# Kernel tuning notes

Measured on AMD Instinct MI355X. Metric: run time of the kernel, lower is better.

## Reference

```python
import jax, jax.numpy as jnp
import numpy as np

V, E, H, OUT, T = 100000, 300, 512, 1, 2048


def setup_inputs() -> dict:
    key = jax.random.key(0)
    ks = jax.random.split(key, 15)
    s = 0.04  # ~1/sqrt(hidden) init scale
    return {
        "sentA": jax.random.randint(ks[0], (T,), 0, V),
        "sentB": jax.random.randint(ks[1], (T,), 0, V),
        "hidden": jnp.zeros((2, 2, H), jnp.float32),  # unused by forward, kept for signature fidelity
        "emb": jax.random.normal(ks[2], (V, E), jnp.float32) * 0.1,
        "w_ih": jax.random.normal(ks[3], (2, 4 * H, E), jnp.float32) * s,
        "w_hh": jax.random.normal(ks[4], (2, 4 * H, H), jnp.float32) * s,
        "b_ih": jax.random.normal(ks[5], (2, 4 * H), jnp.float32) * s,
        "b_hh": jax.random.normal(ks[6], (2, 4 * H), jnp.float32) * s,
        "bi_w": jax.random.uniform(ks[7], (1, 2), jnp.float32, -0.5, 0.5),
        "bi_b": jax.random.normal(ks[8], (1,), jnp.float32) * s,
        "blA": jax.random.uniform(ks[9], (H, H), jnp.float32, -0.1, 0.1),
        "blB": jax.random.uniform(ks[10], (H, H), jnp.float32, -0.1, 0.1),
        "bl_b": jax.random.normal(ks[11], (H,), jnp.float32) * s,
        "out_w": jax.random.uniform(ks[12], (OUT, H), jnp.float32, -0.1, 0.1),
        "out_b": jax.random.normal(ks[13], (OUT,), jnp.float32) * s,
    }


def _lstm_dir(x, w_ih, w_hh, b_ih, b_hh):
    # x: [T, E]; single-direction LSTM, returns final hidden state h_T [H]
    gx = x @ w_ih.T + (b_ih + b_hh)  # [T, 4H] input-gate preactivations, hoisted out of scan
    h_dim = w_hh.shape[1]

    def step(carry, g_t):
        h, c = carry
        g = g_t + h @ w_hh.T  # [4H]
        i, f, gg, o = jnp.split(g, 4, axis=-1)  # PyTorch gate order: i, f, g, o
        c = jax.nn.sigmoid(f) * c + jax.nn.sigmoid(i) * jnp.tanh(gg)
        h = jax.nn.sigmoid(o) * jnp.tanh(c)
        return (h, c), None

    init = (jnp.zeros((h_dim,), x.dtype), jnp.zeros((h_dim,), x.dtype))
    (h, _), _ = jax.lax.scan(step, init, gx)
    return h


def _encode(sent, emb, w_ih, w_hh, b_ih, b_hh, bi_w, bi_b):
    x = emb[sent]  # [T, E]
    h_fwd = _lstm_dir(x, w_ih[0], w_hh[0], b_ih[0], b_hh[0])
    h_bwd = _lstm_dir(x[::-1], w_ih[1], w_hh[1], b_ih[1], b_hh[1])
    hid = jnp.stack([h_fwd, h_bwd])  # [2, H]
    # bi_weight(hid.t()).t(): mixes the 2 directions per hidden unit -> [1, H]
    return bi_w @ hid + bi_b


def reference(sentA, sentB, hidden, emb, w_ih, w_hh, b_ih, b_hh,
              bi_w, bi_b, blA, blB, bl_b, out_w, out_b):
    hA = _encode(sentA, emb, w_ih, w_hh, b_ih, b_hh, bi_w, bi_b)  # [1, H]
    hB = _encode(sentB, emb, w_ih, w_hh, b_ih, b_hh, bi_w, bi_b)  # [1, H]
    # Double_Linear: A @ WA + B @ WB + bias
    biout = hA @ blA + hB @ blB + bl_b  # [1, H]
    out_l = jnp.tanh(biout) @ out_w.T + out_b  # [1, OUT]
    return jax.nn.sigmoid(out_l)
```

## Files before the change

kernel.cpp:

```cpp
#include <hip/hip_runtime.h>
#include <hip/hip_bf16.h>

#define T_LEN 2048
#define E_DIM 300
#define H_DIM 512
#define G_DIM 2048
#define NBLK  32
#define UPB   16
#define TAG_OFF 0x40000000u

#define WS_H   0
#define WS_X   16384
#define WS_GX  5242880

typedef float v2f __attribute__((ext_vector_type(2)));

__device__ __forceinline__ float sigmoid_fast(float x) {
    return 1.f / (1.f + __expf(-x));
}
__device__ __forceinline__ float tanh_fast(float x) {
    x = fminf(fmaxf(x, -15.f), 15.f);
    float e = __expf(-2.f * x);
    return (1.f - e) / (1.f + e);
}

__global__ void k_gather(const int* __restrict__ sentA, const int* __restrict__ sentB,
                         const float* __restrict__ emb, float* __restrict__ x) {
    const int s = blockIdx.y;
    const int* sent = s ? sentB : sentA;
    const int t0 = blockIdx.x * 16;
    for (int idx = threadIdx.x; idx < 16 * 300; idx += 256) {
        int r = idx / 300, e = idx - r * 300;
        int t = t0 + r;
        int row = sent[t];
        x[((size_t)(s * 2048 + t)) * 300 + e] = emb[(size_t)row * 300 + e];
    }
}

__global__ __launch_bounds__(256) void k_gemm(const float* __restrict__ x,
                                              const float* __restrict__ w_ih,
                                              const float* __restrict__ b_ih,
                                              const float* __restrict__ b_hh,
                                              __hip_bfloat16* __restrict__ gx) {
    __shared__ float xs[32 * 108];
    __shared__ float ws_[64 * 108];
    const int gi = blockIdx.x, ti = blockIdx.y, z = blockIdx.z;
    const int d = z >> 1, s = z & 1;
    const int t0 = ti * 32, g0 = gi * 64;
    const int tg = threadIdx.x & 15, tt = threadIdx.x >> 4;
    const float* wbase = w_ih + (size_t)d * G_DIM * E_DIM;

    float acc[2][4];
#pragma unroll
    for (int j = 0; j < 2; ++j)
#pragma unroll
        for (int i = 0; i < 4; ++i) acc[j][i] = 0.f;

    for (int e0 = 0; e0 < 300; e0 += 100) {
        for (int idx = threadIdx.x; idx < 32 * 25; idx += 256) {
            int r = idx / 25, c = idx - r * 25;
            float4 v = *(const float4*)(x + ((size_t)(s * 2048 + t0 + r)) * 300 + e0 + c * 4);
            *(float4*)&xs[r * 108 + c * 4] = v;
        }
        for (int idx = threadIdx.x; idx < 64 * 25; idx += 256) {
            int r = idx / 25, c = idx - r * 25;
            float4 v = *(const float4*)(wbase + (size_t)(g0 + r) * 300 + e0 + c * 4);
            *(float4*)&ws_[r * 108 + c * 4] = v;
        }
        __syncthreads();

        for (int c = 0; c < 25; ++c) {
            float4 xv[2], wv[4];
#pragma unroll
            for (int j = 0; j < 2; ++j) xv[j] = *(const float4*)&xs[(tt + 16 * j) * 108 + c * 4];
#pragma unroll
            for (int i = 0; i < 4; ++i) wv[i] = *(const float4*)&ws_[(tg + 16 * i) * 108 + c * 4];
#pragma unroll
            for (int j = 0; j < 2; ++j)
#pragma unroll
                for (int i = 0; i < 4; ++i)
                    acc[j][i] += xv[j].x * wv[i].x + xv[j].y * wv[i].y +
                                 xv[j].z * wv[i].z + xv[j].w * wv[i].w;
        }
        __syncthreads();
    }

#pragma unroll
    for (int i = 0; i < 4; ++i) {
        int g = g0 + tg + 16 * i;
        float bias = b_ih[d * G_DIM + g] + b_hh[d * G_DIM + g];
        int pos = ((g >> 4) & 31) * 64 + (g >> 9) * 16 + (g & 15);
#pragma unroll
        for (int j = 0; j < 2; ++j) {
            int t = t0 + tt + 16 * j;
            int tout = d ? (T_LEN - 1 - t) : t;
            float v = acc[j][i] + bias;
            gx[(((size_t)(d * 2 + s) * T_LEN + tout) << 11) + pos] = __float2bfloat16(v);
        }
    }
}

__global__ __launch_bounds__(256, 1) void k_rnn(const float* __restrict__ w_hh,
                                                const __hip_bfloat16* __restrict__ gx,
                                                unsigned long long* __restrict__ hb) {
    const int tid  = threadIdx.x;
    const int lane = tid & 63;
    const int w    = tid >> 6;
    const int sub  = tid & 3;
    const int q_g  = (tid >> 2) & 3;
    const int ul_g = tid >> 4;
    const int bid = blockIdx.x;
    const int d  = bid >> 6;
    const int s  = (bid >> 5) & 1;
    const int bb = bid & 31;

    v2f wreg2[8][8];
#pragma unroll
    for (int r2 = 0; r2 < 8; ++r2)
#pragma unroll
        for (int kb = 0; kb < 8; ++kb) {
            const float* wp = w_hh + ((size_t)d * G_DIM + w * 512 + bb * 16 + 2 * r2) * H_DIM
                            + kb * 64 + lane;
            v2f t2; t2.x = wp[0]; t2.y = wp[H_DIM];
            wreg2[r2][kb] = t2;
        }

    __shared__ float hlds[H_DIM];
    __shared__ float pacc[64 * 68];

    float c_state = 0.f;

    if ((lane & 15) == 0) {
        __hip_atomic_store(&hb[((size_t)(d * 2 + 0) * 2 + s) * H_DIM + bb * UPB + ul_g],
                           (unsigned long long)TAG_OFF << 32,
                           __ATOMIC_RELAXED, __HIP_MEMORY_SCOPE_AGENT);
    }

    const int i0 = w * 128 + lane;
    const int i1 = i0 + 64;

    for (int t = 0; t < T_LEN; ++t) {
        const int p  = t & 1;
        const int pn = p ^ 1;

        float gxv = (float)gx[(((size_t)(d * 2 + s) * T_LEN + t) << 11)
                              + bb * 64 + q_g * 16 + ul_g];

        unsigned long long* hbp = hb + ((size_t)(d * 2 + p) * 2 + s) * H_DIM;
        const unsigned int tag = TAG_OFF + (unsigned int)t;
        unsigned long long a0, a1, b0, b1;

#define LDH(X) __hip_atomic_load(&hbp[X], __ATOMIC_RELAXED, __HIP_MEMORY_SCOPE_AGENT)
        a0 = LDH(i0); a1 = LDH(i1);
        int guard = 0;
        for (;;) {
            b0 = LDH(i0); b1 = LDH(i1);
            bool okA = ((unsigned int)(a0 >> 32) == tag) & ((unsigned int)(a1 >> 32) == tag);
            if (__all(okA)) break;
            if (++guard > (1 << 20)) break;
            a0 = LDH(i0); a1 = LDH(i1);
            bool okB = ((unsigned int)(b0 >> 32) == tag) & ((unsigned int)(b1 >> 32) == tag);
            if (__all(okB)) { a0 = b0; a1 = b1; break; }
            if (++guard > (1 << 20)) break;
        }
#undef LDH

        hlds[i0] = __uint_as_float((unsigned int)a0);
        hlds[i1] = __uint_as_float((unsigned int)a1);
        __syncthreads();

        float hv[8];
#pragma unroll
        for (int kb = 0; kb < 8; ++kb)
            hv[kb] = hlds[kb * 64 + lane];

        v2f acc2[8];
#pragma unroll
        for (int r2 = 0; r2 < 8; ++r2) acc2[r2] = (v2f)(0.f);
#pragma unroll
        for (int kb = 0; kb < 8; ++kb) {
            float h0 = hv[kb];
            v2f h2; h2.x = h0; h2.y = h0;
#pragma unroll
            for (int r2 = 0; r2 < 8; ++r2)
                acc2[r2] += wreg2[r2][kb] * h2;
        }

#pragma unroll
        for (int r2 = 0; r2 < 8; ++r2) {
            pacc[((2 * r2 + 0) * 4 + w) * 68 + lane] = acc2[r2].x;
            pacc[((2 * r2 + 1) * 4 + w) * 68 + lane] = acc2[r2].y;
        }
        __syncthreads();

        const float4* pr = (const float4*)&pacc[(tid >> 2) * 68 + sub * 16];
        float4 sv = pr[0];
#pragma unroll
        for (int j2 = 1; j2 < 4; ++j2) {
            float4 q4 = pr[j2];
            sv.x += q4.x; sv.y += q4.y; sv.z += q4.z; sv.w += q4.w;
        }
        float v = (sv.x + sv.y) + (sv.z + sv.w);
        v += __shfl_xor(v, 1, 64);
        v += __shfl_xor(v, 2, 64);
        v += gxv;
        float act = (q_g == 2) ? tanh_fast(v) : sigmoid_fast(v);

        const int g0l = lane & ~15;
        float si = __shfl(act, g0l + 0,  64);
        float sf = __shfl(act, g0l + 4,  64);
        float tg = __shfl(act, g0l + 8,  64);
        float so = __shfl(act, g0l + 12, 64);
        if ((lane & 15) == 0) {
            c_state = sf * c_state + si * tg;
            float h_new = so * tanh_fast(c_state);
            unsigned long long pkt = ((unsigned long long)(TAG_OFF + (unsigned int)(t + 1)) << 32)
                                   | (unsigned long long)__float_as_uint(h_new);
            __hip_atomic_store(&hb[((size_t)(d * 2 + pn) * 2 + s) * H_DIM + bb * UPB + ul_g],
                               pkt, __ATOMIC_RELAXED, __HIP_MEMORY_SCOPE_AGENT);
        }
    }
}

__global__ __launch_bounds__(512) void k_head(const unsigned long long* __restrict__ hb,
                                              const float* __restrict__ bi_w,
                                              const float* __restrict__ bi_b,
                                              const float* __restrict__ blA,
                                              const float* __restrict__ blB,
                                              const float* __restrict__ bl_b,
                                              const float* __restrict__ out_w,
                                              const float* __restrict__ out_b,
                                              float* __restrict__ out) {
    __shared__ float enc[2][512];
    __shared__ float red[8];
    const int tid = threadIdx.x;
    const float bw0 = bi_w[0], bw1 = bi_w[1], bib = bi_b[0];
    {
        int u = tid;
        float hfA = __uint_as_float((unsigned int)hb[((0 * 2 + 0) * 2 + 0) * 512 + u]);
        float hbA = __uint_as_float((unsigned int)hb[((1 * 2 + 0) * 2 + 0) * 512 + u]);
        float hfB = __uint_as_float((unsigned int)hb[((0 * 2 + 0) * 2 + 1) * 512 + u]);
        float hbB = __uint_as_float((unsigned int)hb[((1 * 2 + 0) * 2 + 1) * 512 + u]);
        enc[0][u] = bw0 * hfA + bw1 * hbA + bib;
        enc[1][u] = bw0 * hfB + bw1 * hbB + bib;
    }
    __syncthreads();
    const int j = tid;
    float acc = bl_b[j];
#pragma unroll 4
    for (int u = 0; u < 512; ++u)
        acc += enc[0][u] * blA[u * 512 + j] + enc[1][u] * blB[u * 512 + j];
    float contrib = tanh_fast(acc) * out_w[j];
#pragma unroll
    for (int m = 1; m < 64; m <<= 1) contrib += __shfl_xor(contrib, m, 64);
    if ((tid & 63) == 0) red[tid >> 6] = contrib;
    __syncthreads();
    if (tid == 0) {
        float s = 0.f;
#pragma unroll
        for (int i = 0; i < 8; ++i) s += red[i];
        s += out_b[0];
        out[0] = sigmoid_fast(s);
    }
}

extern "C" void kernel_launch(void* const* d_in, const int* in_sizes, int n_in,
                              void* d_out, int out_size, void* d_ws, size_t ws_size,
                              hipStream_t stream) {
    const int*   sentA = (const int*)d_in[0];
    const int*   sentB = (const int*)d_in[1];
    const float* emb   = (const float*)d_in[3];
    const float* w_ih  = (const float*)d_in[4];
    const float* w_hh  = (const float*)d_in[5];
    const float* b_ih  = (const float*)d_in[6];
    const float* b_hh  = (const float*)d_in[7];
    const float* bi_w  = (const float*)d_in[8];
    const float* bi_b  = (const float*)d_in[9];
    const float* blA   = (const float*)d_in[10];
    const float* blB   = (const float*)d_in[11];
    const float* bl_b  = (const float*)d_in[12];
    const float* out_w = (const float*)d_in[13];
    const float* out_b = (const float*)d_in[14];
    float* out = (float*)d_out;

    char* ws = (char*)d_ws;
    unsigned long long* hbf = (unsigned long long*)(ws + WS_H);
    float*              x   = (float*)(ws + WS_X);
    __hip_bfloat16*     gx  = (__hip_bfloat16*)(ws + WS_GX);

    k_gather<<<dim3(128, 2), 256, 0, stream>>>(sentA, sentB, emb, x);
    k_gemm<<<dim3(32, 64, 4), 256, 0, stream>>>(x, w_ih, b_ih, b_hh, gx);
    k_rnn<<<dim3(128), 256, 0, stream>>>(w_hh, gx, hbf);
    k_head<<<dim3(1), 512, 0, stream>>>(hbf, bi_w, bi_b, blA, blB, bl_b, out_w, out_b, out);
}
```

Before: 4.423 ms.

## Halve recurrent block count with 512-thread blocks and pipelined polling

Reshapes the persistent LSTM recurrence so each of 16 blocks per sequence/direction owns 32 hidden units using 512 threads, instead of 32 blocks of 256 threads each owning 16 units. The gx layout is permuted to match. Each thread now polls a single h entry through a three-deep rolling load pipeline rather than two entries with alternating loads. Fewer participating blocks means fewer producers per cross-block handoff each timestep, which is meant to cut synchronization latency on the serial critical path. The cost is a larger pacc buffer and barriers that span twice as many waves.

```diff
diff --git a/kernel.cpp b/kernel.cpp
--- a/kernel.cpp
+++ b/kernel.cpp
@@ -5,8 +5,8 @@
 #define E_DIM 300
 #define H_DIM 512
 #define G_DIM 2048
-#define NBLK  32
-#define UPB   16
+#define NBLK  16
+#define UPB   32
 #define TAG_OFF 0x40000000u
 
 #define WS_H   0
@@ -89,7 +89,7 @@
     for (int i = 0; i < 4; ++i) {
         int g = g0 + tg + 16 * i;
         float bias = b_ih[d * G_DIM + g] + b_hh[d * G_DIM + g];
-        int pos = ((g >> 4) & 31) * 64 + (g >> 9) * 16 + (g & 15);
+        int pos = ((g >> 5) & 15) * 128 + (g >> 9) * 32 + (g & 31);
 #pragma unroll
         for (int j = 0; j < 2; ++j) {
             int t = t0 + tt + 16 * j;
@@ -100,73 +100,68 @@
     }
 }
 
-__global__ __launch_bounds__(256, 1) void k_rnn(const float* __restrict__ w_hh,
+__global__ __launch_bounds__(512, 1) void k_rnn(const float* __restrict__ w_hh,
                                                 const __hip_bfloat16* __restrict__ gx,
                                                 unsigned long long* __restrict__ hb) {
     const int tid  = threadIdx.x;
     const int lane = tid & 63;
     const int w    = tid >> 6;
+    const int gw   = w >> 1;
+    const int uh   = w & 1;
     const int sub  = tid & 3;
     const int q_g  = (tid >> 2) & 3;
-    const int ul_g = tid >> 4;
+    const int u_g  = tid >> 4;
     const int bid = blockIdx.x;
-    const int d  = bid >> 6;
-    const int s  = (bid >> 5) & 1;
-    const int bb = bid & 31;
+    const int d  = bid >> 5;
+    const int s  = (bid >> 4) & 1;
+    const int bb = bid & 15;
 
     v2f wreg2[8][8];
 #pragma unroll
     for (int r2 = 0; r2 < 8; ++r2)
 #pragma unroll
         for (int kb = 0; kb < 8; ++kb) {
-            const float* wp = w_hh + ((size_t)d * G_DIM + w * 512 + bb * 16 + 2 * r2) * H_DIM
+            const float* wp = w_hh + ((size_t)d * G_DIM + gw * 512 + bb * 32 + uh * 16 + 2 * r2) * H_DIM
                             + kb * 64 + lane;
             v2f t2; t2.x = wp[0]; t2.y = wp[H_DIM];
             wreg2[r2][kb] = t2;
         }
 
     __shared__ float hlds[H_DIM];
-    __shared__ float pacc[64 * 68];
+    __shared__ float pacc[128 * 68];
 
     float c_state = 0.f;
 
-    if ((lane & 15) == 0) {
-        __hip_atomic_store(&hb[((size_t)(d * 2 + 0) * 2 + s) * H_DIM + bb * UPB + ul_g],
+    if ((tid & 15) == 0) {
+        __hip_atomic_store(&hb[((size_t)(d * 2 + 0) * 2 + s) * H_DIM + bb * UPB + u_g],
                            (unsigned long long)TAG_OFF << 32,
                            __ATOMIC_RELAXED, __HIP_MEMORY_SCOPE_AGENT);
     }
 
-    const int i0 = w * 128 + lane;
-    const int i1 = i0 + 64;
+    const int i0 = w * 64 + lane;
 
     for (int t = 0; t < T_LEN; ++t) {
         const int p  = t & 1;
         const int pn = p ^ 1;
 
         float gxv = (float)gx[(((size_t)(d * 2 + s) * T_LEN + t) << 11)
-                              + bb * 64 + q_g * 16 + ul_g];
+                              + bb * 128 + q_g * 32 + u_g];
 
         unsigned long long* hbp = hb + ((size_t)(d * 2 + p) * 2 + s) * H_DIM;
         const unsigned int tag = TAG_OFF + (unsigned int)t;
-        unsigned long long a0, a1, b0, b1;
-
-#define LDH(X) __hip_atomic_load(&hbp[X], __ATOMIC_RELAXED, __HIP_MEMORY_SCOPE_AGENT)
-        a0 = LDH(i0); a1 = LDH(i1);
+
+#define LDH() __hip_atomic_load(&hbp[i0], __ATOMIC_RELAXED, __HIP_MEMORY_SCOPE_AGENT)
+        unsigned long long a = LDH();
+        unsigned long long b = LDH();
+        unsigned long long c = LDH();
         int guard = 0;
-        for (;;) {
-            b0 = LDH(i0); b1 = LDH(i1);
-            bool okA = ((unsigned int)(a0 >> 32) == tag) & ((unsigned int)(a1 >> 32) == tag);
-            if (__all(okA)) break;
-            if (++guard > (1 << 20)) break;
-            a0 = LDH(i0); a1 = LDH(i1);
-            bool okB = ((unsigned int)(b0 >> 32) == tag) & ((unsigned int)(b1 >> 32) == tag);
-            if (__all(okB)) { a0 = b0; a1 = b1; break; }
-            if (++guard > (1 << 20)) break;
+        while (!__all((unsigned int)(a >> 32) == tag)) {
+            a = b; b = c; c = LDH();
+            if (++guard > (1 << 21)) break;
         }
 #undef LDH
 
-        hlds[i0] = __uint_as_float((unsigned int)a0);
-        hlds[i1] = __uint_as_float((unsigned int)a1);
+        hlds[i0] = __uint_as_float((unsigned int)a);
         __syncthreads();
 
         float hv[8];
@@ -188,8 +183,8 @@
 
 #pragma unroll
         for (int r2 = 0; r2 < 8; ++r2) {
-            pacc[((2 * r2 + 0) * 4 + w) * 68 + lane] = acc2[r2].x;
-            pacc[((2 * r2 + 1) * 4 + w) * 68 + lane] = acc2[r2].y;
+            pacc[((uh * 16 + 2 * r2 + 0) * 4 + gw) * 68 + lane] = acc2[r2].x;
+            pacc[((uh * 16 + 2 * r2 + 1) * 4 + gw) * 68 + lane] = acc2[r2].y;
         }
         __syncthreads();
 
@@ -211,12 +206,12 @@
         float sf = __shfl(act, g0l + 4,  64);
         float tg = __shfl(act, g0l + 8,  64);
         float so = __shfl(act, g0l + 12, 64);
-        if ((lane & 15) == 0) {
+        if ((tid & 15) == 0) {
             c_state = sf * c_state + si * tg;
             float h_new = so * tanh_fast(c_state);
             unsigned long long pkt = ((unsigned long long)(TAG_OFF + (unsigned int)(t + 1)) << 32)
                                    | (unsigned long long)__float_as_uint(h_new);
-            __hip_atomic_store(&hb[((size_t)(d * 2 + pn) * 2 + s) * H_DIM + bb * UPB + ul_g],
+            __hip_atomic_store(&hb[((size_t)(d * 2 + pn) * 2 + s) * H_DIM + bb * UPB + u_g],
                                pkt, __ATOMIC_RELAXED, __HIP_MEMORY_SCOPE_AGENT);
         }
     }
@@ -290,6 +285,6 @@
 
     k_gather<<<dim3(128, 2), 256, 0, stream>>>(sentA, sentB, emb, x);
     k_gemm<<<dim3(32, 64, 4), 256, 0, stream>>>(x, w_ih, b_ih, b_hh, gx);
-    k_rnn<<<dim3(128), 256, 0, stream>>>(w_hh, gx, hbf);
+    k_rnn<<<dim3(64), 512, 0, stream>>>(w_hh, gx, hbf);
     k_head<<<dim3(1), 512, 0, stream>>>(hbf, bi_w, bi_b, blA, blB, bl_b, out_w, out_b, out);
 }
```

After: 5.835 ms. +31.9%, slower.

## Pack two bf16 hidden values per tagged 64-bit exchange word

Applied to the files above, without the earlier changes.

The hidden-state exchange between blocks now stores two units' h values as bf16 in the low 32 bits of each tagged 64-bit word, halving the number of atomic words polled per step. Each lane spins on one word instead of two, which is meant to cut the latency of the per-timestep cross-block handoff. h is rounded to bf16 on every recurrence step, so error can accumulate over 2048 steps. The head kernel decodes the same packed format.

```diff
diff --git a/kernel.cpp b/kernel.cpp
--- a/kernel.cpp
+++ b/kernel.cpp
@@ -22,6 +22,15 @@
     x = fminf(fmaxf(x, -15.f), 15.f);
     float e = __expf(-2.f * x);
     return (1.f - e) / (1.f + e);
+}
+__device__ __forceinline__ unsigned int bf16bits(float x) {
+    __hip_bfloat16 h = __float2bfloat16(x);
+    unsigned short u;
+    __builtin_memcpy(&u, &h, 2);
+    return (unsigned int)u;
+}
+__device__ __forceinline__ float bf16val(unsigned int bits16) {
+    return __uint_as_float(bits16 << 16);
 }
 
 __global__ void k_gather(const int* __restrict__ sentA, const int* __restrict__ sentB,
@@ -130,14 +139,13 @@
 
     float c_state = 0.f;
 
-    if ((lane & 15) == 0) {
-        __hip_atomic_store(&hb[((size_t)(d * 2 + 0) * 2 + s) * H_DIM + bb * UPB + ul_g],
+    if ((tid & 31) == 0) {
+        __hip_atomic_store(&hb[((size_t)(d * 2 + 0) * 2 + s) * 256 + bb * 8 + (ul_g >> 1)],
                            (unsigned long long)TAG_OFF << 32,
                            __ATOMIC_RELAXED, __HIP_MEMORY_SCOPE_AGENT);
     }
 
-    const int i0 = w * 128 + lane;
-    const int i1 = i0 + 64;
+    const int i0 = w * 64 + lane;
 
     for (int t = 0; t < T_LEN; ++t) {
         const int p  = t & 1;
@@ -146,27 +154,28 @@
         float gxv = (float)gx[(((size_t)(d * 2 + s) * T_LEN + t) << 11)
                               + bb * 64 + q_g * 16 + ul_g];
 
-        unsigned long long* hbp = hb + ((size_t)(d * 2 + p) * 2 + s) * H_DIM;
+        unsigned long long* hbp = hb + ((size_t)(d * 2 + p) * 2 + s) * 256;
         const unsigned int tag = TAG_OFF + (unsigned int)t;
-        unsigned long long a0, a1, b0, b1;
-
-#define LDH(X) __hip_atomic_load(&hbp[X], __ATOMIC_RELAXED, __HIP_MEMORY_SCOPE_AGENT)
-        a0 = LDH(i0); a1 = LDH(i1);
+        unsigned long long a0, b0;
+
+#define LDH() __hip_atomic_load(&hbp[i0], __ATOMIC_RELAXED, __HIP_MEMORY_SCOPE_AGENT)
+        a0 = LDH();
         int guard = 0;
         for (;;) {
-            b0 = LDH(i0); b1 = LDH(i1);
-            bool okA = ((unsigned int)(a0 >> 32) == tag) & ((unsigned int)(a1 >> 32) == tag);
-            if (__all(okA)) break;
+            b0 = LDH();
+            if (__all((unsigned int)(a0 >> 32) == tag)) break;
             if (++guard > (1 << 20)) break;
-            a0 = LDH(i0); a1 = LDH(i1);
-            bool okB = ((unsigned int)(b0 >> 32) == tag) & ((unsigned int)(b1 >> 32) == tag);
-            if (__all(okB)) { a0 = b0; a1 = b1; break; }
+            a0 = LDH();
+            if (__all((unsigned int)(b0 >> 32) == tag)) { a0 = b0; break; }
             if (++guard > (1 << 20)) break;
         }
 #undef LDH
 
-        hlds[i0] = __uint_as_float((unsigned int)a0);
-        hlds[i1] = __uint_as_float((unsigned int)a1);
+        {
+            unsigned int lo = (unsigned int)a0;
+            hlds[2 * i0 + 0] = bf16val(lo & 0xffffu);
+            hlds[2 * i0 + 1] = bf16val(lo >> 16);
+        }
         __syncthreads();
 
         float hv[8];
@@ -211,12 +220,17 @@
         float sf = __shfl(act, g0l + 4,  64);
         float tg = __shfl(act, g0l + 8,  64);
         float so = __shfl(act, g0l + 12, 64);
-        if ((lane & 15) == 0) {
-            c_state = sf * c_state + si * tg;
-            float h_new = so * tanh_fast(c_state);
-            unsigned long long pkt = ((unsigned long long)(TAG_OFF + (unsigned int)(t + 1)) << 32)
-                                   | (unsigned long long)__float_as_uint(h_new);
-            __hip_atomic_store(&hb[((size_t)(d * 2 + pn) * 2 + s) * H_DIM + bb * UPB + ul_g],
+
+        c_state = sf * c_state + si * tg;
+        float h_new = so * tanh_fast(c_state);
+        float h_pair = __shfl(h_new, (lane + 16) & 63, 64);
+
+        if ((tid & 31) == 0) {
+            unsigned long long pkt =
+                ((unsigned long long)(TAG_OFF + (unsigned int)(t + 1)) << 32)
+                | ((unsigned long long)bf16bits(h_pair) << 16)
+                | (unsigned long long)bf16bits(h_new);
+            __hip_atomic_store(&hb[((size_t)(d * 2 + pn) * 2 + s) * 256 + bb * 8 + (ul_g >> 1)],
                                pkt, __ATOMIC_RELAXED, __HIP_MEMORY_SCOPE_AGENT);
         }
     }
@@ -237,10 +251,11 @@
     const float bw0 = bi_w[0], bw1 = bi_w[1], bib = bi_b[0];
     {
         int u = tid;
-        float hfA = __uint_as_float((unsigned int)hb[((0 * 2 + 0) * 2 + 0) * 512 + u]);
-        float hbA = __uint_as_float((unsigned int)hb[((1 * 2 + 0) * 2 + 0) * 512 + u]);
-        float hfB = __uint_as_float((unsigned int)hb[((0 * 2 + 0) * 2 + 1) * 512 + u]);
-        float hbB = __uint_as_float((unsigned int)hb[((1 * 2 + 0) * 2 + 1) * 512 + u]);
+        int pk = u >> 1, sh = (u & 1) * 16;
+        float hfA = bf16val((unsigned int)((hb[(size_t)(0 * 2 + 0) * 2 * 256 + 0 * 256 + pk] >> sh) & 0xffffu));
+        float hbA = bf16val((unsigned int)((hb[(size_t)(1 * 2 + 0) * 2 * 256 + 0 * 256 + pk] >> sh) & 0xffffu));
+        float hfB = bf16val((unsigned int)((hb[(size_t)(0 * 2 + 0) * 2 * 256 + 1 * 256 + pk] >> sh) & 0xffffu));
+        float hbB = bf16val((unsigned int)((hb[(size_t)(1 * 2 + 0) * 2 * 256 + 1 * 256 + pk] >> sh) & 0xffffu));
         enc[0][u] = bw0 * hfA + bw1 * hbA + bib;
         enc[1][u] = bw0 * hfB + bw1 * hbB + bib;
     }
```

Result: slower. 4.718 ms (+6.6%).

## Replicate hidden-state broadcast buffers per block to spread polling traffic

Applied to the files above, without the earlier changes.

Each recurrent block now polls its own private double-buffered copy of the hidden-state vector instead of one shared buffer per chain. Producers write each new h value into all 32 block replicas, with lanes spread across the copies, and every lane now computes the cell update. The aim is to cut contention and cache-line ping-pong from 32 blocks spinning on the same addresses. The cost is 32x more store traffic per step and a larger workspace, which shifts the offsets of the other buffers.

```diff
diff --git a/kernel.cpp b/kernel.cpp
--- a/kernel.cpp
+++ b/kernel.cpp
@@ -10,8 +10,8 @@
 #define TAG_OFF 0x40000000u
 
 #define WS_H   0
-#define WS_X   16384
-#define WS_GX  5242880
+#define WS_X   2097152
+#define WS_GX  7012352
 
 typedef float v2f __attribute__((ext_vector_type(2)));
 
@@ -113,6 +113,7 @@
     const int d  = bid >> 6;
     const int s  = (bid >> 5) & 1;
     const int bb = bid & 31;
+    const int cs = d * 2 + s;
 
     v2f wreg2[8][8];
 #pragma unroll
@@ -130,23 +131,27 @@
 
     float c_state = 0.f;
 
-    if ((lane & 15) == 0) {
-        __hip_atomic_store(&hb[((size_t)(d * 2 + 0) * 2 + s) * H_DIM + bb * UPB + ul_g],
-                           (unsigned long long)TAG_OFF << 32,
-                           __ATOMIC_RELAXED, __HIP_MEMORY_SCOPE_AGENT);
-    }
+    unsigned long long* myreg = hb + (((size_t)cs * 32 + bb) * 2) * 512;
+
+    __hip_atomic_store(&myreg[2 * tid + 0], (unsigned long long)TAG_OFF << 32,
+                       __ATOMIC_RELAXED, __HIP_MEMORY_SCOPE_AGENT);
+    __hip_atomic_store(&myreg[2 * tid + 1], (unsigned long long)TAG_OFF << 32,
+                       __ATOMIC_RELAXED, __HIP_MEMORY_SCOPE_AGENT);
 
     const int i0 = w * 128 + lane;
     const int i1 = i0 + 64;
+
+    const int rrep = tid & 15;
+    const int gu   = bb * 16 + ul_g;
 
     for (int t = 0; t < T_LEN; ++t) {
         const int p  = t & 1;
         const int pn = p ^ 1;
 
-        float gxv = (float)gx[(((size_t)(d * 2 + s) * T_LEN + t) << 11)
+        float gxv = (float)gx[(((size_t)cs * T_LEN + t) << 11)
                               + bb * 64 + q_g * 16 + ul_g];
 
-        unsigned long long* hbp = hb + ((size_t)(d * 2 + p) * 2 + s) * H_DIM;
+        unsigned long long* hbp = myreg + (size_t)p * 512;
         const unsigned int tag = TAG_OFF + (unsigned int)t;
         unsigned long long a0, a1, b0, b1;
 
@@ -211,13 +216,18 @@
         float sf = __shfl(act, g0l + 4,  64);
         float tg = __shfl(act, g0l + 8,  64);
         float so = __shfl(act, g0l + 12, 64);
-        if ((lane & 15) == 0) {
-            c_state = sf * c_state + si * tg;
-            float h_new = so * tanh_fast(c_state);
-            unsigned long long pkt = ((unsigned long long)(TAG_OFF + (unsigned int)(t + 1)) << 32)
-                                   | (unsigned long long)__float_as_uint(h_new);
-            __hip_atomic_store(&hb[((size_t)(d * 2 + pn) * 2 + s) * H_DIM + bb * UPB + ul_g],
-                               pkt, __ATOMIC_RELAXED, __HIP_MEMORY_SCOPE_AGENT);
+
+        c_state = sf * c_state + si * tg;
+        float h_new = so * tanh_fast(c_state);
+        unsigned long long pkt = ((unsigned long long)(TAG_OFF + (unsigned int)(t + 1)) << 32)
+                               | (unsigned long long)__float_as_uint(h_new);
+
+        {
+            unsigned long long* base = hb + (size_t)cs * 32 * 2 * 512 + (size_t)pn * 512 + gu;
+            __hip_atomic_store(base + (size_t)rrep * 1024, pkt,
+                               __ATOMIC_RELAXED, __HIP_MEMORY_SCOPE_AGENT);
+            __hip_atomic_store(base + (size_t)(rrep + 16) * 1024, pkt,
+                               __ATOMIC_RELAXED, __HIP_MEMORY_SCOPE_AGENT);
         }
     }
 }
@@ -237,10 +247,10 @@
     const float bw0 = bi_w[0], bw1 = bi_w[1], bib = bi_b[0];
     {
         int u = tid;
-        float hfA = __uint_as_float((unsigned int)hb[((0 * 2 + 0) * 2 + 0) * 512 + u]);
-        float hbA = __uint_as_float((unsigned int)hb[((1 * 2 + 0) * 2 + 0) * 512 + u]);
-        float hfB = __uint_as_float((unsigned int)hb[((0 * 2 + 0) * 2 + 1) * 512 + u]);
-        float hbB = __uint_as_float((unsigned int)hb[((1 * 2 + 0) * 2 + 1) * 512 + u]);
+        float hfA = __uint_as_float((unsigned int)hb[(size_t)0 * 32768 + u]);
+        float hfB = __uint_as_float((unsigned int)hb[(size_t)1 * 32768 + u]);
+        float hbA = __uint_as_float((unsigned int)hb[(size_t)2 * 32768 + u]);
+        float hbB = __uint_as_float((unsigned int)hb[(size_t)3 * 32768 + u]);
         enc[0][u] = bw0 * hfA + bw1 * hbA + bib;
         enc[1][u] = bw0 * hfB + bw1 * hbB + bib;
     }
```

Result: slower. 5.087 ms (+15.0%).
